# Kernel tuning notes

Measured on AMD Instinct MI355X. Metric: run time of the kernel, lower is better.

Reference implementation:

```python
import jax, jax.numpy as jnp
import numpy as np
from jax import lax

B, N, M, NCLS = 16, 8192, 64, 80          # batch, anchors, GT boxes, classes
M_W, M_H = 640, 640                       # config.model_in_sz
CLASS_ID = 0                              # config.objective_class_id
PROB_T = 0.0                              # prob_threshold default
IOU_MATCH = 0.5                           # GT<->pred matching threshold
NMS_THR = 0.5                             # NMS IoU threshold
EPS = 1e-7


def xywh2xyxy(x):
    cx, cy, w, h = x[..., 0], x[..., 1], x[..., 2], x[..., 3]
    return jnp.stack([cx - w / 2, cy - h / 2, cx + w / 2, cy + h / 2], axis=-1)


def box_iou(a, b):
    # torchvision-style IoU (no +1), a: (M,4), b: (N,4) -> (M,N)
    area_a = (a[:, 2] - a[:, 0]) * (a[:, 3] - a[:, 1])
    area_b = (b[:, 2] - b[:, 0]) * (b[:, 3] - b[:, 1])
    lt = jnp.maximum(a[:, None, :2], b[None, :, :2])
    rb = jnp.minimum(a[:, None, 2:], b[None, :, 2:])
    wh = jnp.clip(rb - lt, 0)
    inter = wh[..., 0] * wh[..., 1]
    return inter / (area_a[:, None] + area_b[None, :] - inter)


def setup_inputs() -> dict:
    key = jax.random.key(0)
    k1, k2, k3, k4, k5 = jax.random.split(key, 5)
    # GT labels: [class_id, cx, cy, w, h] normalized to [0,1]
    cxy = jax.random.uniform(k1, (B, M, 2), minval=0.2, maxval=0.8)
    wh = jax.random.uniform(k2, (B, M, 2), minval=0.05, maxval=0.25)
    cls = jnp.zeros((B, M, 1), jnp.float32)
    label_batch = jnp.concatenate([cls, cxy, wh], axis=-1)  # (B, M, 5)
    # Predictions: each anchor is a GT box (pixel xywh) + small noise, so
    # IoU>=0.5 matching and NMS actually fire.
    gt_idx = jnp.arange(N) % M
    scale = jnp.array([M_W, M_H, M_W, M_H], jnp.float32)
    base = label_batch[:, gt_idx, 1:] * scale               # (B, N, 4)
    pred_xywh = base + jax.random.normal(k3, (B, N, 4)) * 2.0
    obj = jax.random.uniform(k4, (B, N, 1), minval=0.1, maxval=1.0)
    cls_logits = jax.random.uniform(k5, (B, N, NCLS))
    output = jnp.concatenate([pred_xywh, obj, cls_logits], axis=-1)  # (B,N,85)
    return {"output": output, "label_batch": label_batch}


def nms_keep(boxes, scores, valid):
    # Greedy NMS over a padded candidate set. `valid` marks real candidates;
    # invalid entries get -inf score and can never suppress anything.
    n = boxes.shape[0]
    order = jnp.argsort(jnp.where(valid, scores, -jnp.inf))[::-1]
    b = boxes[order]
    v = valid[order]
    x1, y1, x2, y2 = b[:, 0], b[:, 1], b[:, 2], b[:, 3]
    area = (x2 - x1 + 1) * (y2 - y1 + 1)   # +1 convention, as in the source nms
    pos = jnp.arange(n)

    def body(i, supp):
        active = v[i] & jnp.logical_not(supp[i])
        xx1 = jnp.maximum(x1[i], x1)
        yy1 = jnp.maximum(y1[i], y1)
        xx2 = jnp.minimum(x2[i], x2)
        yy2 = jnp.minimum(y2[i], y2)
        inter = jnp.clip(xx2 - xx1 + 1, 0) * jnp.clip(yy2 - yy1 + 1, 0)
        iou = inter / (area[i] + area - inter + EPS)
        return supp | (active & (pos > i) & (iou > NMS_THR))

    supp = lax.fori_loop(0, n, body, jnp.zeros(n, dtype=bool))
    return v & jnp.logical_not(supp), order


def _per_image(out, lab):
    pred_boxes = xywh2xyxy(out[:, :4])                      # (N,4) pixel xyxy
    obj = out[:, 4]
    logits = out[:, 5 + CLASS_ID] * obj                     # class prob * objectness
    scale = jnp.array([M_W, M_H, M_W, M_H], out.dtype)
    gt = jnp.clip(xywh2xyxy(lab[:, 1:]), 0, 1) * scale      # (M,4) pixel xyxy
    iou = box_iou(gt, pred_boxes)                           # (M,N)
    # candidate = passes prob threshold AND overlaps some GT with IoU>=0.5
    valid = (obj >= PROB_T) & jnp.any(iou >= IOU_MATCH, axis=0)
    keep, order = nms_keep(lax.stop_gradient(pred_boxes),
                           lax.stop_gradient(logits), valid)
    kept = keep.astype(out.dtype)
    return jnp.sum(logits[order] * kept) / jnp.sum(kept)


def reference(output, label_batch):
    loss = jax.vmap(_per_image)(output, label_batch)        # (B,)
    return loss[None, :]                                    # (1, B)
```

## Files before the change

### kernel.cpp

```cpp
#include <hip/hip_runtime.h>
#include <math.h>

#define BB 16
#define NN 8192
#define MM 64
#define ROW 85
#define EPS_F 1e-7f

#define NT1 256
#define NT2 1024
#define NW  16
#define CPW 4
#define CAPB 8

typedef unsigned long long u64;

__global__ void prep_kernel(const float* __restrict__ outp,
                            const float* __restrict__ lab,
                            float4* __restrict__ boxes,
                            float* __restrict__ keys) {
    __shared__ float4 gbox[MM];
    __shared__ float garea[MM];
    const int b = blockIdx.x;
    const int tid = threadIdx.x;
    if (tid < MM) {
        const float* lr = lab + ((size_t)b * MM + tid) * 5;
        float cx = lr[1], cy = lr[2], w = lr[3], h = lr[4];
        float x1 = fminf(fmaxf(cx - w * 0.5f, 0.f), 1.f) * 640.f;
        float y1 = fminf(fmaxf(cy - h * 0.5f, 0.f), 1.f) * 640.f;
        float x2 = fminf(fmaxf(cx + w * 0.5f, 0.f), 1.f) * 640.f;
        float y2 = fminf(fmaxf(cy + h * 0.5f, 0.f), 1.f) * 640.f;
        gbox[tid] = make_float4(x1, y1, x2, y2);
        garea[tid] = (x2 - x1) * (y2 - y1);
    }
    __syncthreads();
    const int n = blockIdx.y * NT1 + tid;
    const float* row = outp + ((size_t)b * NN + n) * ROW;
    float cx = row[0], cy = row[1], w = row[2], h = row[3];
    float obj = row[4], c0 = row[5];
    float px1 = cx - w * 0.5f, py1 = cy - h * 0.5f;
    float px2 = cx + w * 0.5f, py2 = cy + h * 0.5f;
    float pa = (px2 - px1) * (py2 - py1);

    const int m0 = n & (MM - 1);
    bool match;
    {
        float4 g = gbox[m0];
        float iw = fmaxf(fminf(px2, g.z) - fmaxf(px1, g.x), 0.f);
        float ih = fmaxf(fminf(py2, g.w) - fmaxf(py1, g.y), 0.f);
        float inter = iw * ih;
        match = (inter / (garea[m0] + pa - inter) >= 0.5f);
    }
    if (!match) {
        for (int m = 0; m < MM; ++m) {
            float4 g = gbox[m];
            float iw = fmaxf(fminf(px2, g.z) - fmaxf(px1, g.x), 0.f);
            float ih = fmaxf(fminf(py2, g.w) - fmaxf(py1, g.y), 0.f);
            float inter = iw * ih;
            match = match || (inter / (garea[m] + pa - inter) >= 0.5f);
        }
    }
    bool valid = (obj >= 0.0f) && match;
    size_t bn = (size_t)b * NN + ((n & 63) * 128 + (n >> 6));
    boxes[bn] = make_float4(px1, py1, px2, py2);
    keys[bn] = valid ? (c0 * obj) : -INFINITY;
}

__device__ __forceinline__ float wave_fold_max(float x) {
#define DPP_STEPX(ctrl)                                                          \
    { int _o = __builtin_amdgcn_update_dpp(__float_as_int(x), __float_as_int(x), \
                                           (ctrl), 0xF, 0xF, false);             \
      x = fmaxf(x, __int_as_float(_o)); }
    DPP_STEPX(0x111) DPP_STEPX(0x112) DPP_STEPX(0x114)
    DPP_STEPX(0x118) DPP_STEPX(0x142) DPP_STEPX(0x143)
#undef DPP_STEPX
    return x;
}
__device__ __forceinline__ float wave_fold_min(float x) {
#define DPP_STEPN(ctrl)                                                          \
    { int _o = __builtin_amdgcn_update_dpp(__float_as_int(x), __float_as_int(x), \
                                           (ctrl), 0xF, 0xF, false);             \
      x = fminf(x, __int_as_float(_o)); }
    DPP_STEPN(0x111) DPP_STEPN(0x112) DPP_STEPN(0x114)
    DPP_STEPN(0x118) DPP_STEPN(0x142) DPP_STEPN(0x143)
#undef DPP_STEPN
    return x;
}
__device__ __forceinline__ float wave_max64(float x) {
    return __int_as_float(__builtin_amdgcn_readlane(__float_as_int(wave_fold_max(x)), 63));
}
__device__ __forceinline__ float wave_sum64(float x) {
#define DPP_ADD(ctrl)                                                            \
    { int _o = __builtin_amdgcn_update_dpp(0, __float_as_int(x),                 \
                                           (ctrl), 0xF, 0xF, true);              \
      x += __int_as_float(_o); }
    DPP_ADD(0x111) DPP_ADD(0x112) DPP_ADD(0x114)
    DPP_ADD(0x118) DPP_ADD(0x142) DPP_ADD(0x143)
#undef DPP_ADD
    return __int_as_float(__builtin_amdgcn_readlane(__float_as_int(x), 63));
}
__device__ __forceinline__ float bcastlane(float v, int l) {
    return __int_as_float(__builtin_amdgcn_readlane(__float_as_int(v), l));
}

#define KILL_TEST(AK, K_)  do {                                                  \
    float _xx1 = fmaxf(bj.x, lx1[K_]), _yy1 = fmaxf(bj.y, ly1[K_]);              \
    float _xx2 = fminf(bj.z, lx2[K_]), _yy2 = fminf(bj.w, ly2[K_]);              \
    float _iw = fmaxf(_xx2 - _xx1 + 1.f, 0.f);                                   \
    float _ih = fmaxf(_yy2 - _yy1 + 1.f, 0.f);                                   \
    float _in = _iw * _ih;                                                       \
    if (sj > lps[K_] && 1.5f * _in > hbj + lha[K_]) (AK) = -INFINITY;            \
} while (0)

#define DO_CLUSTER(C_) do {                                                      \
    const int c = (C_);                                                          \
                       \
    int _i0 = c * 128 + lane;                                                    \
    float4 _bb0 = boxes[base + _i0];                                             \
    float4 _bb1 = boxes[base + _i0 + 64];                                        \
    float  _k0  = keys[base + _i0];                                              \
    float  _k1  = keys[base + _i0 + 64];                                         \
    u64 om0 = kMask0[c], om1 = kMask1[c];                                        \
    float4 CBc = clusterBB[c];                                                   \
    float mha = 0.5f * clusterMinA[c];                                           \
                     \
    bool _flag = false;                                                          \
    {                                                                            \
        const u64 _adjc = adjL[c];                                               \
        if ((_adjc >> lane) & 1ull) {                                            \
            int _K = keptCnt[lane];                                              \
            if (_K > CAPB) _flag = true;                                         \
            int _KB = _K < CAPB ? _K : CAPB;                                     \
            _Pragma("unroll 4")                                                  \
            for (int _t2 = 0; _t2 < _KB; ++_t2) {                                \
                float4 _bj = keptBoxL[lane][_t2];                                \
                float2 _mt = keptMetaL[lane][_t2];                               \
                float _iwS = fminf(_bj.z, CBc.z) - fmaxf(_bj.x, CBc.x) + 1.f;    \
                float _ihS = fminf(_bj.w, CBc.w) - fmaxf(_bj.y, CBc.y) + 1.f;    \
                if (_iwS > 0.f && _ihS > 0.f && 1.5f * (_iwS * _ihS) > _mt.y + mha) \
                    _flag = true;                                                \
            }                                                                    \
        }                                                                        \
    }                                                                            \
    u64 passM = __ballot(_flag);                                                 \
                                                  \
    float lx1[2] = { _bb0.x, _bb1.x }, ly1[2] = { _bb0.y, _bb1.y };              \
    float lx2[2] = { _bb0.z, _bb1.z }, ly2[2] = { _bb0.w, _bb1.w };              \
    float lps[2] = { _k0, _k1 };                                                 \
    float lha[2] = { 0.5f * ((lx2[0] - lx1[0] + 1.f) * (ly2[0] - ly1[0] + 1.f)), \
                     0.5f * ((lx2[1] - lx1[1] + 1.f) * (ly2[1] - ly1[1] + 1.f)) };\
    float a0 = lps[0], a1 = lps[1];                                              \
                                         \
    while (passM) {                                                              \
        int ac = __ffsll(passM) - 1; passM &= (passM - 1);                       \
        int K = keptCnt[ac];                                                     \
        int KB = K < CAPB ? K : CAPB;                                            \
        _Pragma("unroll 4")                                                      \
        for (int t2 = 0; t2 < KB; ++t2) {                                        \
            float4 bj = keptBoxL[ac][t2];                                        \
            float2 mt = keptMetaL[ac][t2];                                       \
            float iwS = fminf(bj.z, CBc.z) - fmaxf(bj.x, CBc.x) + 1.f;           \
            float ihS = fminf(bj.w, CBc.w) - fmaxf(bj.y, CBc.y) + 1.f;           \
            if (iwS > 0.f && ihS > 0.f && 1.5f * (iwS * ihS) > mt.y + mha) {     \
                float sj = mt.x, hbj = mt.y;                                     \
                KILL_TEST(a0, 0);                                                \
                KILL_TEST(a1, 1);                                                \
            }                                                                    \
        }                                                                        \
        if (K > CAPB) {                               \
            u64 mm = kMask0[ac];                                                 \
            while (mm) {                                                         \
                int bit = __ffsll(mm) - 1; mm &= (mm - 1);                       \
                int gi = ac * 128 + bit;                                         \
                float4 bj = boxes[base + gi];                                    \
                float sj = keys[base + gi];                                      \
                float hbj = 0.5f * ((bj.z - bj.x + 1.f) * (bj.w - bj.y + 1.f))   \
                            + 0.5f * EPS_F;                                      \
                KILL_TEST(a0, 0);                                                \
                KILL_TEST(a1, 1);                                                \
            }                                                                    \
            mm = kMask1[ac];                                                     \
            while (mm) {                                                         \
                int bit = __ffsll(mm) - 1; mm &= (mm - 1);                       \
                int gi = ac * 128 + 64 + bit;                                    \
                float4 bj = boxes[base + gi];                                    \
                float sj = keys[base + gi];                                      \
                float hbj = 0.5f * ((bj.z - bj.x + 1.f) * (bj.w - bj.y + 1.f))   \
                            + 0.5f * EPS_F;                                      \
                KILL_TEST(a0, 0);                                                \
                KILL_TEST(a1, 1);                                                \
            }                                                                    \
        }                                                                        \
    }                                                                            \
                              \
    bool kept0 = false, kept1 = false;                                           \
    int cnt = 0;                                                                 \
    while (true) {                                                               \
        float lv = fmaxf(a0, a1);                                                \
        float wm = wave_max64(lv);                                               \
        if (wm == -INFINITY) break;                                              \
        u64 bm = __ballot(lv == wm);                                             \
        int wl = __ffsll(bm) - 1;                                                \
        int la = (a0 == lv) ? 0 : 1;                                             \
        float cxa = la ? lx1[1] : lx1[0];                                        \
        float cya = la ? ly1[1] : ly1[0];                                        \
        float cxb = la ? lx2[1] : lx2[0];                                        \
        float cyb = la ? ly2[1] : ly2[0];                                        \
        float cha = la ? lha[1] : lha[0];                                        \
        float bx1 = bcastlane(cxa, wl), by1 = bcastlane(cya, wl);                \
        float bx2 = bcastlane(cxb, wl), by2 = bcastlane(cyb, wl);                \
        float hcb = bcastlane(cha, wl) + 0.5f * EPS_F;                           \
        if (lane == wl) {                                                        \
            if (cnt < CAPB) {                                                    \
                keptBoxL[c][cnt] = make_float4(cxa, cya, cxb, cyb);              \
                keptMetaL[c][cnt] = make_float2(lv, cha + 0.5f * EPS_F);         \
            }                                                                    \
            if (la == 0) { kept0 = true; a0 = -INFINITY; }                       \
            else         { kept1 = true; a1 = -INFINITY; }                       \
        }                                                                        \
        cnt++;                                                                   \
        if (a0 != -INFINITY) {                                                   \
            float xx1 = fmaxf(bx1, lx1[0]), yy1 = fmaxf(by1, ly1[0]);            \
            float xx2 = fminf(bx2, lx2[0]), yy2 = fminf(by2, ly2[0]);            \
            float iw = fmaxf(xx2 - xx1 + 1.f, 0.f);                              \
            float ih = fmaxf(yy2 - yy1 + 1.f, 0.f);                              \
            if (1.5f * (iw * ih) > hcb + lha[0]) a0 = -INFINITY;                 \
        }                                                                        \
        if (a1 != -INFINITY) {                                                   \
            float xx1 = fmaxf(bx1, lx1[1]), yy1 = fmaxf(by1, ly1[1]);            \
            float xx2 = fminf(bx2, lx2[1]), yy2 = fminf(by2, ly2[1]);            \
            float iw = fmaxf(xx2 - xx1 + 1.f, 0.f);                              \
            float ih = fmaxf(yy2 - yy1 + 1.f, 0.f);                              \
            if (1.5f * (iw * ih) > hcb + lha[1]) a1 = -INFINITY;                 \
        }                                                                        \
    }                                                                            \
    u64 m0 = __ballot(kept0);                                                    \
    u64 m1 = __ballot(kept1);                                                    \
    if (lane == 0) {                                                             \
        kMask0[c] = m0; kMask1[c] = m1; keptCnt[c] = cnt;                        \
        if (m0 != om0 || m1 != om1)                                              \
            atomicOr(&chMask[nxt][c >> 5], 1u << (c & 31));                      \
    }                                                                            \
} while (0)

__global__ void __launch_bounds__(NT2)
nms_kernel(const float4* __restrict__ boxes, const float* __restrict__ keys,
           float* __restrict__ loss) {
    __shared__ float4 clusterBB[MM];
    __shared__ float  clusterMinA[MM];
    __shared__ float  topScore[MM];
    __shared__ int    slotCluster[MM];
    __shared__ u64    adjL[MM];
    __shared__ float4 keptBoxL[MM][CAPB];
    __shared__ float2 keptMetaL[MM][CAPB];
    __shared__ u64    kMask0[MM];
    __shared__ u64    kMask1[MM];
    __shared__ int    keptCnt[MM];
    __shared__ unsigned int chMask[3][2];
    __shared__ float  waveSum[NW];
    __shared__ int    waveCnt[NW];

    const int b = blockIdx.x;
    const int tid = threadIdx.x;
    const int wid = tid >> 6;
    const int lane = tid & 63;
    const size_t base = (size_t)b * NN;

#pragma unroll
    for (int q = 0; q < CPW; ++q) {
        const int c = CPW * wid + q;
        float mx = INFINITY, my = INFINITY, Mx = -INFINITY, My = -INFINITY;
        float mA = INFINITY, tS = -INFINITY;
#pragma unroll
        for (int s = 0; s < 2; ++s) {
            int idx = c * 128 + s * 64 + lane;
            float4 bb = boxes[base + idx];
            float sc = keys[base + idx];
            float ar = (bb.z - bb.x + 1.f) * (bb.w - bb.y + 1.f);
            if (sc != -INFINITY) {
                mx = fminf(mx, bb.x); my = fminf(my, bb.y);
                Mx = fmaxf(Mx, bb.z); My = fmaxf(My, bb.w);
                mA = fminf(mA, ar);   tS = fmaxf(tS, sc);
            }
        }
        mx = wave_fold_min(mx); my = wave_fold_min(my);
        Mx = wave_fold_max(Mx); My = wave_fold_max(My);
        mA = wave_fold_min(mA); tS = wave_fold_max(tS);
        if (lane == 63) {
            clusterBB[c] = make_float4(mx, my, Mx, My);
            clusterMinA[c] = mA;
            topScore[c] = tS;
        }
    }
    __syncthreads();

    if (wid == 0) {
        const int t = lane;
        float4 bbT = clusterBB[t];
        float  maT = clusterMinA[t];
        u64 adj = 0ull;
        for (int j = 0; j < MM; ++j) {
            float4 bbJ = clusterBB[j];
            float  maJ = clusterMinA[j];
            float iw = fminf(bbT.z, bbJ.z) - fmaxf(bbT.x, bbJ.x) + 1.f;
            float ih = fminf(bbT.w, bbJ.w) - fmaxf(bbT.y, bbJ.y) + 1.f;
            if (j != t && iw > 0.f && ih > 0.f) {
                float I = iw * ih;
                bool noe = (3.f * I < maT + maJ) || (2.f * I < fmaxf(maT, maJ));
                if (!noe) adj |= (1ull << j);
            }
        }
        adjL[t] = adj;
        kMask0[t] = 0ull; kMask1[t] = 0ull;
        keptCnt[t] = 0;
        float myS = topScore[t];
        int r = 0;
        for (int j = 0; j < MM; ++j) {
            float sj = topScore[j];
            r += (sj > myS || (sj == myS && j < t)) ? 1 : 0;
        }
        slotCluster[r] = t;
        if (t == 0) {
            chMask[0][0] = 0xFFFFFFFFu; chMask[0][1] = 0xFFFFFFFFu;
            chMask[1][0] = 0u; chMask[1][1] = 0u;
            chMask[2][0] = 0u; chMask[2][1] = 0u;
        }
    }
    __syncthreads();

    int cq[CPW];
#pragma unroll
    for (int q = 0; q < CPW; ++q) cq[q] = slotCluster[q * NW + wid];

    for (int rr = 0; rr < 8200; ++rr) {
        const int cur = rr % 3, nxt = (rr + 1) % 3, clr = (rr + 2) % 3;
        const u64 cm = ((u64)chMask[cur][1] << 32) | (u64)chMask[cur][0];
        if (cm == 0ull) break;
        if (tid == 0) { chMask[clr][0] = 0u; chMask[clr][1] = 0u; }
#pragma unroll
        for (int q = 0; q < CPW; ++q) {
            const int c1 = cq[q];
            if (((adjL[c1] | (1ull << c1)) & cm) == 0ull) continue;
            DO_CLUSTER(c1);
        }
#pragma unroll
        for (int q = 0; q < CPW; ++q) {
            const int c2 = cq[q];
            const u64 g2 = ((u64)chMask[nxt][1] << 32) | (u64)chMask[nxt][0];
            if ((adjL[c2] & g2) == 0ull) continue;
            DO_CLUSTER(c2);
        }
        __syncthreads();
    }

    float s = 0.f; int ccount = 0;
#pragma unroll
    for (int q = 0; q < CPW; ++q) {
        const int c = cq[q];
        u64 m0 = kMask0[c], m1 = kMask1[c];
        if ((m0 >> lane) & 1ull) s += keys[base + c * 128 + lane];
        if ((m1 >> lane) & 1ull) s += keys[base + c * 128 + 64 + lane];
        ccount += (int)__popcll(m0) + (int)__popcll(m1);
    }
    s = wave_sum64(s);
    if (lane == 0) { waveSum[wid] = s; waveCnt[wid] = ccount; }
    __syncthreads();
    if (tid == 0) {
        float tot = 0.f; int ct = 0;
#pragma unroll
        for (int w = 0; w < NW; ++w) { tot += waveSum[w]; ct += waveCnt[w]; }
        loss[b] = tot / (float)ct;
    }
}

extern "C" void kernel_launch(void* const* d_in, const int* in_sizes, int n_in,
                              void* d_out, int out_size, void* d_ws, size_t ws_size,
                              hipStream_t stream) {
    const float* outp = (const float*)d_in[0];
    const float* lab  = (const float*)d_in[1];
    float* loss = (float*)d_out;

    float4* boxes = (float4*)d_ws;
    float*  keys  = (float*)((char*)d_ws + (size_t)BB * NN * sizeof(float4));

    dim3 g1(BB, NN / NT1);
    prep_kernel<<<g1, NT1, 0, stream>>>(outp, lab, boxes, keys);
    nms_kernel<<<BB, NT2, 0, stream>>>(boxes, keys, loss);
}
```

Before: 62.35 us.

## Double-buffer cluster keep state and propagate precise dirty targets per round

The iterative cluster NMS fixpoint now keeps its kept-box state in two parity buffers (Jacobi-style) instead of updating in place with a second Gauss-Seidel pass per round. When a cluster's keep mask changes, it tests only the changed boxes against neighbouring cluster bounding boxes and marks just the clusters they could affect as dirty. Clean clusters copy their state forward. This aims to skip redundant cluster re-evaluations, but dropping the in-round second pass may need more rounds to converge and adds copy traffic.

```diff
diff --git a/kernel.cpp b/kernel.cpp
--- a/kernel.cpp
+++ b/kernel.cpp
@@ -112,6 +112,21 @@
     if (sj > lps[K_] && 1.5f * _in > hbj + lha[K_]) (AK) = -INFINITY;            \
 } while (0)
 
+#define PUSH_DELTA(DD, SLOT) do {                                                \
+    u64 _dd = (DD);                                                              \
+    while (_dd) {                                                                \
+        int _j = __ffsll(_dd) - 1; _dd &= (_dd - 1);                             \
+        float _ex1 = bcastlane(lx1[SLOT], _j), _ey1 = bcastlane(ly1[SLOT], _j);  \
+        float _ex2 = bcastlane(lx2[SLOT], _j), _ey2 = bcastlane(ly2[SLOT], _j);  \
+        float _eha = bcastlane(lha[SLOT], _j);                                   \
+        float _iwp = fminf(_ex2, tbL.z) - fmaxf(_ex1, tbL.x) + 1.f;              \
+        float _ihp = fminf(_ey2, tbL.w) - fmaxf(_ey1, tbL.y) + 1.f;              \
+        bool _hit = (_iwp > 0.f) && (_ihp > 0.f) &&                              \
+                    (1.5f * (_iwp * _ihp) > _eha + 0.5f * EPS_F + tmhaL);        \
+        targets |= __ballot(_hit);                                               \
+    }                                                                            \
+} while (0)
+
 #define DO_CLUSTER(C_) do {                                                      \
     const int c = (C_);                                                          \
                        \
@@ -120,7 +135,7 @@
     float4 _bb1 = boxes[base + _i0 + 64];                                        \
     float  _k0  = keys[base + _i0];                                              \
     float  _k1  = keys[base + _i0 + 64];                                         \
-    u64 om0 = kMask0[c], om1 = kMask1[c];                                        \
+    u64 om0 = kMask0[par][c], om1 = kMask1[par][c];                              \
     float4 CBc = clusterBB[c];                                                   \
     float mha = 0.5f * clusterMinA[c];                                           \
                      \
@@ -128,13 +143,13 @@
     {                                                                            \
         const u64 _adjc = adjL[c];                                               \
         if ((_adjc >> lane) & 1ull) {                                            \
-            int _K = keptCnt[lane];                                              \
+            int _K = keptCnt[par][lane];                                         \
             if (_K > CAPB) _flag = true;                                         \
             int _KB = _K < CAPB ? _K : CAPB;                                     \
             _Pragma("unroll 4")                                                  \
             for (int _t2 = 0; _t2 < _KB; ++_t2) {                                \
-                float4 _bj = keptBoxL[lane][_t2];                                \
-                float2 _mt = keptMetaL[lane][_t2];                               \
+                float4 _bj = keptBoxL[par][lane][_t2];                           \
+                float2 _mt = keptMetaL[par][lane][_t2];                          \
                 float _iwS = fminf(_bj.z, CBc.z) - fmaxf(_bj.x, CBc.x) + 1.f;    \
                 float _ihS = fminf(_bj.w, CBc.w) - fmaxf(_bj.y, CBc.y) + 1.f;    \
                 if (_iwS > 0.f && _ihS > 0.f && 1.5f * (_iwS * _ihS) > _mt.y + mha) \
@@ -153,12 +168,12 @@
                                          \
     while (passM) {                                                              \
         int ac = __ffsll(passM) - 1; passM &= (passM - 1);                       \
-        int K = keptCnt[ac];                                                     \
+        int K = keptCnt[par][ac];                                                \
         int KB = K < CAPB ? K : CAPB;                                            \
         _Pragma("unroll 4")                                                      \
         for (int t2 = 0; t2 < KB; ++t2) {                                        \
-            float4 bj = keptBoxL[ac][t2];                                        \
-            float2 mt = keptMetaL[ac][t2];                                       \
+            float4 bj = keptBoxL[par][ac][t2];                                   \
+            float2 mt = keptMetaL[par][ac][t2];                                  \
             float iwS = fminf(bj.z, CBc.z) - fmaxf(bj.x, CBc.x) + 1.f;           \
             float ihS = fminf(bj.w, CBc.w) - fmaxf(bj.y, CBc.y) + 1.f;           \
             if (iwS > 0.f && ihS > 0.f && 1.5f * (iwS * ihS) > mt.y + mha) {     \
@@ -168,7 +183,7 @@
             }                                                                    \
         }                                                                        \
         if (K > CAPB) {                               \
-            u64 mm = kMask0[ac];                                                 \
+            u64 mm = kMask0[par][ac];                                            \
             while (mm) {                                                         \
                 int bit = __ffsll(mm) - 1; mm &= (mm - 1);                       \
                 int gi = ac * 128 + bit;                                         \
@@ -179,7 +194,7 @@
                 KILL_TEST(a0, 0);                                                \
                 KILL_TEST(a1, 1);                                                \
             }                                                                    \
-            mm = kMask1[ac];                                                     \
+            mm = kMask1[par][ac];                                                \
             while (mm) {                                                         \
                 int bit = __ffsll(mm) - 1; mm &= (mm - 1);                       \
                 int gi = ac * 128 + 64 + bit;                                    \
@@ -192,7 +207,7 @@
             }                                                                    \
         }                                                                        \
     }                                                                            \
-                              \
+           \
     bool kept0 = false, kept1 = false;                                           \
     int cnt = 0;                                                                 \
     while (true) {                                                               \
@@ -212,8 +227,8 @@
         float hcb = bcastlane(cha, wl) + 0.5f * EPS_F;                           \
         if (lane == wl) {                                                        \
             if (cnt < CAPB) {                                                    \
-                keptBoxL[c][cnt] = make_float4(cxa, cya, cxb, cyb);              \
-                keptMetaL[c][cnt] = make_float2(lv, cha + 0.5f * EPS_F);         \
+                keptBoxL[parN][c][cnt] = make_float4(cxa, cya, cxb, cyb);        \
+                keptMetaL[parN][c][cnt] = make_float2(lv, cha + 0.5f * EPS_F);   \
             }                                                                    \
             if (la == 0) { kept0 = true; a0 = -INFINITY; }                       \
             else         { kept1 = true; a1 = -INFINITY; }                       \
@@ -237,9 +252,33 @@
     u64 m0 = __ballot(kept0);                                                    \
     u64 m1 = __ballot(kept1);                                                    \
     if (lane == 0) {                                                             \
-        kMask0[c] = m0; kMask1[c] = m1; keptCnt[c] = cnt;                        \
-        if (m0 != om0 || m1 != om1)                                              \
-            atomicOr(&chMask[nxt][c >> 5], 1u << (c & 31));                      \
+        kMask0[parN][c] = m0; kMask1[parN][c] = m1; keptCnt[parN][c] = cnt;      \
+    }                                                                            \
+    u64 d0 = m0 ^ om0, d1 = m1 ^ om1;                                            \
+    if ((d0 | d1) != 0ull) {                                                     \
+        float4 tbL = clusterBB[lane];                                            \
+        float tmhaL = 0.5f * clusterMinA[lane];                                  \
+        u64 targets = 0ull;                                                      \
+        PUSH_DELTA(d0, 0);                                                       \
+        PUSH_DELTA(d1, 1);                                                       \
+        targets &= adjL[c];                                                      \
+        if (lane == 0 && targets) {                                              \
+            atomicOr(&dirtyM[nxt][0], (unsigned)(targets & 0xffffffffull));      \
+            atomicOr(&dirtyM[nxt][1], (unsigned)(targets >> 32));                \
+        }                                                                        \
+    }                                                                            \
+} while (0)
+
+#define COPY_CLUSTER(C_) do {                                                    \
+    const int c = (C_);                                                          \
+    if (lane < CAPB) {                                                           \
+        keptBoxL[parN][c][lane] = keptBoxL[par][c][lane];                        \
+        keptMetaL[parN][c][lane] = keptMetaL[par][c][lane];                      \
+    }                                                                            \
+    if (lane == 0) {                                                             \
+        kMask0[parN][c] = kMask0[par][c];                                        \
+        kMask1[parN][c] = kMask1[par][c];                                        \
+        keptCnt[parN][c] = keptCnt[par][c];                                      \
     }                                                                            \
 } while (0)
 
@@ -251,12 +290,12 @@
     __shared__ float  topScore[MM];
     __shared__ int    slotCluster[MM];
     __shared__ u64    adjL[MM];
-    __shared__ float4 keptBoxL[MM][CAPB];
-    __shared__ float2 keptMetaL[MM][CAPB];
-    __shared__ u64    kMask0[MM];
-    __shared__ u64    kMask1[MM];
-    __shared__ int    keptCnt[MM];
-    __shared__ unsigned int chMask[3][2];
+    __shared__ float4 keptBoxL[2][MM][CAPB];
+    __shared__ float2 keptMetaL[2][MM][CAPB];
+    __shared__ u64    kMask0[2][MM];
+    __shared__ u64    kMask1[2][MM];
+    __shared__ int    keptCnt[2][MM];
+    __shared__ unsigned int dirtyM[3][2];
     __shared__ float  waveSum[NW];
     __shared__ int    waveCnt[NW];
 
@@ -311,8 +350,8 @@
             }
         }
         adjL[t] = adj;
-        kMask0[t] = 0ull; kMask1[t] = 0ull;
-        keptCnt[t] = 0;
+        kMask0[0][t] = 0ull; kMask1[0][t] = 0ull;
+        keptCnt[0][t] = 0;
         float myS = topScore[t];
         int r = 0;
         for (int j = 0; j < MM; ++j) {
@@ -321,9 +360,9 @@
         }
         slotCluster[r] = t;
         if (t == 0) {
-            chMask[0][0] = 0xFFFFFFFFu; chMask[0][1] = 0xFFFFFFFFu;
-            chMask[1][0] = 0u; chMask[1][1] = 0u;
-            chMask[2][0] = 0u; chMask[2][1] = 0u;
+            dirtyM[0][0] = 0xFFFFFFFFu; dirtyM[0][1] = 0xFFFFFFFFu;
+            dirtyM[1][0] = 0u; dirtyM[1][1] = 0u;
+            dirtyM[2][0] = 0u; dirtyM[2][1] = 0u;
         }
     }
     __syncthreads();
@@ -332,32 +371,31 @@
 #pragma unroll
     for (int q = 0; q < CPW; ++q) cq[q] = slotCluster[q * NW + wid];
 
+    int par = 0;
     for (int rr = 0; rr < 8200; ++rr) {
         const int cur = rr % 3, nxt = (rr + 1) % 3, clr = (rr + 2) % 3;
-        const u64 cm = ((u64)chMask[cur][1] << 32) | (u64)chMask[cur][0];
-        if (cm == 0ull) break;
-        if (tid == 0) { chMask[clr][0] = 0u; chMask[clr][1] = 0u; }
+        const u64 dirty = ((u64)dirtyM[cur][1] << 32) | (u64)dirtyM[cur][0];
+        if (dirty == 0ull) break;
+        if (tid == 0) { dirtyM[clr][0] = 0u; dirtyM[clr][1] = 0u; }
+        const int parN = par ^ 1;
 #pragma unroll
         for (int q = 0; q < CPW; ++q) {
-            const int c1 = cq[q];
-            if (((adjL[c1] | (1ull << c1)) & cm) == 0ull) continue;
-            DO_CLUSTER(c1);
-        }
-#pragma unroll
-        for (int q = 0; q < CPW; ++q) {
-            const int c2 = cq[q];
-            const u64 g2 = ((u64)chMask[nxt][1] << 32) | (u64)chMask[nxt][0];
-            if ((adjL[c2] & g2) == 0ull) continue;
-            DO_CLUSTER(c2);
+            const int cc = cq[q];
+            if ((dirty >> cc) & 1ull) {
+                DO_CLUSTER(cc);
+            } else {
+                COPY_CLUSTER(cc);
+            }
         }
         __syncthreads();
+        par = parN;
     }
 
     float s = 0.f; int ccount = 0;
 #pragma unroll
     for (int q = 0; q < CPW; ++q) {
         const int c = cq[q];
-        u64 m0 = kMask0[c], m1 = kMask1[c];
+        u64 m0 = kMask0[par][c], m1 = kMask1[par][c];
         if ((m0 >> lane) & 1ull) s += keys[base + c * 128 + lane];
         if ((m1 >> lane) & 1ull) s += keys[base + c * 128 + 64 + lane];
         ccount += (int)__popcll(m0) + (int)__popcll(m1);
```

Measured after the change: 63.79 us. 1.02x slower.
